# Kernel tuning notes

Hardware: AMD Instinct MI355X
Metric: run time of the kernel (lower is better)

The kernel has to match this reference:

```python
import jax, jax.numpy as jnp
import numpy as np

LAYERS = [1024, 2048, 1024]
OPTIONS = 4
BATCH = 2048


def setup_inputs() -> dict:
    key = jax.random.key(0)
    k_x, k_idx, k_w1, k_w2 = jax.random.split(key, 4)
    x = jax.random.normal(k_x, (BATCH, LAYERS[0]), dtype=jnp.float32)
    idx = jax.random.randint(k_idx, (BATCH,), 0, OPTIONS, dtype=jnp.int64)
    # xavier-normal-ish scaled weights per layer: shape [options, in, out]
    std1 = float(np.sqrt(2.0 / (LAYERS[0] * LAYERS[1] + OPTIONS * LAYERS[1])))
    std2 = float(np.sqrt(2.0 / (LAYERS[1] * LAYERS[2] + OPTIONS * LAYERS[2])))
    W1 = jax.random.normal(k_w1, (OPTIONS, LAYERS[0], LAYERS[1]), dtype=jnp.float32) * std1
    b1 = jnp.zeros((OPTIONS, LAYERS[1]), dtype=jnp.float32)
    W2 = jax.random.normal(k_w2, (OPTIONS, LAYERS[1], LAYERS[2]), dtype=jnp.float32) * std2
    b2 = jnp.zeros((OPTIONS, LAYERS[2]), dtype=jnp.float32)
    return {"x": x, "idx": idx, "W1": W1, "b1": b1, "W2": W2, "b2": b2}


def reference(x, idx, W1, b1, W2, b2):
    # Original: torch.bmm(x[:,None,:], W[idx]) + b[zeros_like(idx)]
    # Equivalent math without materializing the [B, in, out] gathered weights:
    # compute all options densely, then select per-sample option with idx.
    # NOTE: bias is ALWAYS option 0 (faithful to the original's zeros_like(idx)).
    def layer(h, W, b):
        h_all = jnp.einsum('bi,oij->boj', h, W)  # [B, O, out]
        h_sel = jnp.take_along_axis(h_all, idx[:, None, None], axis=1)[:, 0, :]  # [B, out]
        return h_sel + b[0][None, :]

    h = layer(x, W1, b1)
    out = layer(h, W2, b2)
    return out
```

## Files before the change

kernel.cpp:

```cpp
#include <hip/hip_runtime.h>
#include <stdint.h>

typedef __bf16 bf16x8 __attribute__((ext_vector_type(8)));
typedef float f32x4 __attribute__((ext_vector_type(4)));
typedef unsigned short u16;
typedef const __attribute__((address_space(1))) void* as1_cvp;
typedef __attribute__((address_space(3))) void* as3_vp;

__device__ __forceinline__ u16 f2bf(float f) {
  union { float f; unsigned u; } v; v.f = f;
  unsigned r = v.u + 0x7fffu + ((v.u >> 16) & 1u);
  return (u16)(r >> 16);
}

__global__ __launch_bounds__(256) void hist_perm_kernel(
    const int* __restrict__ idx, int n, int* __restrict__ starts,
    int* __restrict__ perm, int* __restrict__ tmap128,
    int* __restrict__ tmap64) {
  __shared__ int cnt[4][256];
  __shared__ int gtot[4], gstart[4];
  const int t = threadIdx.x;
  const int rpt = (n + 255) >> 8;
  const int base = t * rpt;
  int c[4] = {0, 0, 0, 0};
  for (int j = 0; j < rpt; ++j) {
    const int i = base + j;
    if (i < n) c[idx[i] & 3]++;
  }
  #pragma unroll
  for (int g = 0; g < 4; ++g) cnt[g][t] = c[g];
  __syncthreads();

  const int w = t >> 6, l = t & 63;
  {
    const int s0 = cnt[w][l * 4 + 0], s1 = cnt[w][l * 4 + 1];
    const int s2 = cnt[w][l * 4 + 2], s3 = cnt[w][l * 4 + 3];
    const int sum = s0 + s1 + s2 + s3;
    int sc = sum;
    #pragma unroll
    for (int d = 1; d < 64; d <<= 1) {
      const int o = __shfl_up(sc, d, 64);
      if (l >= d) sc += o;
    }
    const int ex = sc - sum;
    cnt[w][l * 4 + 0] = ex;
    cnt[w][l * 4 + 1] = ex + s0;
    cnt[w][l * 4 + 2] = ex + s0 + s1;
    cnt[w][l * 4 + 3] = ex + s0 + s1 + s2;
    if (l == 63) gtot[w] = sc;
  }
  __syncthreads();

  if (t == 0) {
    int s = 0, nt128 = 0, nt64 = 0;
    for (int g = 0; g < 4; ++g) {
      gstart[g] = s;
      starts[g] = s;
      const int cg = gtot[g];
      for (int j = 0; j < cg; j += 128) tmap128[nt128++] = (g << 28) | (s + j);
      for (int j = 0; j < cg; j += 64)  tmap64[nt64++]  = (g << 28) | (s + j);
      s += cg;
    }
    starts[4] = s;
    while (nt128 < 20) tmap128[nt128++] = -1;
    while (nt64 < 40)  tmap64[nt64++]  = -1;
  }
  __syncthreads();

  int run[4] = {0, 0, 0, 0};
  for (int j = 0; j < rpt; ++j) {
    const int i = base + j;
    if (i < n) {
      const int g = idx[i] & 3;
      perm[gstart[g] + cnt[g][t] + run[g]] = i;
      run[g]++;
    }
  }
}

__global__ __launch_bounds__(256) void prep_kernel(
    const float* __restrict__ W1, u16* __restrict__ W1T,
    const float* __restrict__ W2, u16* __restrict__ W2T,
    const float* __restrict__ x, const int* __restrict__ perm,
    u16* __restrict__ Xs) {
  __shared__ float tile[64][65];
  int bid = blockIdx.x;
  if (bid >= 4096) {
    const int p = bid - 4096;
    const int b = perm[p];
    const float4 v = ((const float4*)(x + (size_t)b * 1024))[threadIdx.x];
    ushort4 u;
    u.x = f2bf(v.x); u.y = f2bf(v.y); u.z = f2bf(v.z); u.w = f2bf(v.w);
    ((ushort4*)(Xs + (size_t)p * 1024))[threadIdx.x] = u;
    return;
  }
  const float* W; u16* WT; int K, N, tx, ty, o;
  if (bid < 2048) {
    W = W1; WT = W1T; K = 1024; N = 2048;
    o = bid >> 9; const int t = bid & 511; tx = t & 31; ty = t >> 5;
  } else {
    bid -= 2048;
    W = W2; WT = W2T; K = 2048; N = 1024;
    o = bid >> 9; const int t = bid & 511; tx = t & 15; ty = t >> 4;
  }
  const float* Wo = W + (size_t)o * K * N;
  u16* WTo = WT + (size_t)o * N * K;
  const int k0 = ty * 64, n0 = tx * 64;
  const int rr = threadIdx.x >> 4, cc = threadIdx.x & 15;
  #pragma unroll
  for (int j = 0; j < 4; ++j) {
    const int r = j * 16 + rr;
    const float4 v = *(const float4*)(Wo + (size_t)(k0 + r) * N + n0 + cc * 4);
    tile[r][cc * 4 + 0] = v.x; tile[r][cc * 4 + 1] = v.y;
    tile[r][cc * 4 + 2] = v.z; tile[r][cc * 4 + 3] = v.w;
  }
  __syncthreads();
  #pragma unroll
  for (int j = 0; j < 4; ++j) {
    const int nrow = j * 16 + rr;
    ushort4 u;
    u.x = f2bf(tile[cc * 4 + 0][nrow]);
    u.y = f2bf(tile[cc * 4 + 1][nrow]);
    u.z = f2bf(tile[cc * 4 + 2][nrow]);
    u.w = f2bf(tile[cc * 4 + 3][nrow]);
    *(ushort4*)(WTo + (size_t)(n0 + nrow) * K + k0 + cc * 4) = u;
  }
}

template <int EPI, int TM, int NT_PAD, int KT, int NN, int NTN>
__global__ __launch_bounds__(256, 2) void gemm_kernel(
    const u16* __restrict__ A, const u16* __restrict__ BT,
    const float* __restrict__ bias, const int* __restrict__ starts,
    const int* __restrict__ tmap, const int* __restrict__ perm,
    u16* __restrict__ outH, float* __restrict__ outF) {
  constexpr int MR = TM / 32;
  constexpr int ABUF = TM * 128;
  constexpr int BSTR = ABUF + 16384;
  __shared__ char smem[2 * BSTR];

  const int nwg = NT_PAD * NTN;
  const int q = nwg >> 3;
  const int bid = blockIdx.x;
  const int swz = (bid & 7) * q + (bid >> 3);
  const int tile = swz % NT_PAD;
  const int n_t = swz / NT_PAD;

  const int tm = tmap[tile];
  if (tm < 0) return;
  const int o = tm >> 28;
  const int m_start = tm & 0x0FFFFFFF;
  const int g1 = starts[o + 1];
  const int n_start = n_t * 128;
  const u16* Bo = BT + (size_t)o * NN * KT;

  const int tid = threadIdx.x;
  const int w = tid >> 6;
  const int l = tid & 63;
  const int wm = w >> 1, wn = w & 1;
  const int l8 = l & 7, ld8 = l >> 3;

  const int src_unit = l8 ^ (ld8 & 7);

  const u16* pA[MR];
  #pragma unroll
  for (int j = 0; j < MR; ++j) {
    int r = m_start + (j * 4 + w) * 8 + ld8;
    if (r >= g1) r = g1 - 1;
    pA[j] = A + (size_t)r * KT + src_unit * 8;
  }
  const u16* pB[4];
  #pragma unroll
  for (int j = 0; j < 4; ++j) {
    const int nr = n_start + (j * 4 + w) * 8 + ld8;
    pB[j] = Bo + (size_t)nr * KT + src_unit * 8;
  }

#define STAGE(dst_off)                                                         \
  {                                                                            \
    _Pragma("unroll")                                                          \
    for (int j = 0; j < MR; ++j)                                               \
      __builtin_amdgcn_global_load_lds((as1_cvp)pA[j],                         \
          (as3_vp)(smem + (dst_off) + (j * 4 + w) * 1024), 16, 0, 0);          \
    _Pragma("unroll")                                                          \
    for (int j = 0; j < 4; ++j)                                                \
      __builtin_amdgcn_global_load_lds((as1_cvp)pB[j],                         \
          (as3_vp)(smem + (dst_off) + ABUF + (j * 4 + w) * 1024), 16, 0, 0);   \
    _Pragma("unroll") for (int j = 0; j < MR; ++j) pA[j] += 64;                \
    _Pragma("unroll") for (int j = 0; j < 4; ++j) pB[j] += 64;                 \
  }

  const int lrow = l & 15;
  const int lx = l & 7;
  const int lu = l >> 4;
  int offA[MR][2], offB[4][2];
  #pragma unroll
  for (int a = 0; a < MR; ++a)
    #pragma unroll
    for (int kk = 0; kk < 2; ++kk)
      offA[a][kk] = (wm * (TM / 2) + a * 16 + lrow) * 128 + (((kk * 4 + lu) ^ lx) << 4);
  #pragma unroll
  for (int b = 0; b < 4; ++b)
    #pragma unroll
    for (int kk = 0; kk < 2; ++kk)
      offB[b][kk] = (wn * 64 + b * 16 + lrow) * 128 + (((kk * 4 + lu) ^ lx) << 4);

  f32x4 acc[MR][4] = {};

  const int nK = KT >> 6;
  STAGE(0);
  for (int kt = 0; kt < nK; ++kt) {
    const int cur = (kt & 1) * BSTR;
    if (kt + 1 < nK) {
      STAGE(BSTR - cur);
      if constexpr (TM == 128)
        asm volatile("s_waitcnt vmcnt(8)" ::: "memory");
      else
        asm volatile("s_waitcnt vmcnt(6)" ::: "memory");
    } else {
      asm volatile("s_waitcnt vmcnt(0)" ::: "memory");
    }
    __builtin_amdgcn_s_barrier();

    bf16x8 af[MR][2], bfr[4][2];
    #pragma unroll
    for (int a = 0; a < MR; ++a)
      #pragma unroll
      for (int kk = 0; kk < 2; ++kk)
        af[a][kk] = *(const bf16x8*)(smem + cur + offA[a][kk]);
    #pragma unroll
    for (int b = 0; b < 4; ++b)
      #pragma unroll
      for (int kk = 0; kk < 2; ++kk)
        bfr[b][kk] = *(const bf16x8*)(smem + cur + ABUF + offB[b][kk]);
    asm volatile("s_waitcnt lgkmcnt(0)" ::: "memory");
    __builtin_amdgcn_s_barrier();

    __builtin_amdgcn_s_setprio(1);
    #pragma unroll
    for (int kk = 0; kk < 2; ++kk)
      #pragma unroll
      for (int a = 0; a < MR; ++a)
        #pragma unroll
        for (int b = 0; b < 4; ++b)
          acc[a][b] = __builtin_amdgcn_mfma_f32_16x16x32_bf16(af[a][kk], bfr[b][kk], acc[a][b], 0, 0, 0);
    __builtin_amdgcn_s_setprio(0);
  }
#undef STAGE

  const int col_l = l & 15;
  const int row_l = (l >> 4) << 2;
  #pragma unroll
  for (int a = 0; a < MR; ++a) {
    #pragma unroll
    for (int b = 0; b < 4; ++b) {
      const int n = n_start + wn * 64 + b * 16 + col_l;
      const float bv = bias[n];
      #pragma unroll
      for (int r = 0; r < 4; ++r) {
        const int p = m_start + wm * (TM / 2) + a * 16 + row_l + r;
        if (p < g1) {
          if (EPI == 0) {
            outH[(size_t)p * NN + n] = f2bf(acc[a][b][r] + bv);
          } else {
            outF[(size_t)perm[p] * NN + n] = acc[a][b][r] + bv;
          }
        }
      }
    }
  }
}

extern "C" void kernel_launch(void* const* d_in, const int* in_sizes, int n_in,
                              void* d_out, int out_size, void* d_ws, size_t ws_size,
                              hipStream_t stream) {
  (void)n_in; (void)out_size; (void)ws_size;
  const float* x   = (const float*)d_in[0];
  const int*   idx = (const int*)d_in[1];
  const float* W1  = (const float*)d_in[2];
  const float* b1  = (const float*)d_in[3];
  const float* W2  = (const float*)d_in[4];
  const float* b2  = (const float*)d_in[5];
  float* out = (float*)d_out;

  const int B = in_sizes[1];

  char* ws = (char*)d_ws;
  u16* W1T     = (u16*)(ws);
  u16* W2T     = (u16*)(ws + 16777216);
  u16* Xs      = (u16*)(ws + 33554432);
  u16* Hs      = (u16*)(ws + 37748736);
  int* perm    = (int*)(ws + 46137344);
  int* starts  = (int*)(ws + 46137344 + 8192);
  int* tmap128 = starts + 64;
  int* tmap64  = starts + 128;

  hist_perm_kernel<<<1, 256, 0, stream>>>(idx, B, starts, perm, tmap128, tmap64);
  prep_kernel<<<4096 + B, 256, 0, stream>>>(W1, W1T, W2, W2T, x, perm, Xs);

  gemm_kernel<0, 128, 20, 1024, 2048, 16><<<320, 256, 0, stream>>>(
      Xs, W1T, b1, starts, tmap128, perm, Hs, nullptr);
  gemm_kernel<1, 64, 40, 2048, 1024, 8><<<320, 256, 0, stream>>>(
      Hs, W2T, b2, starts, tmap64, perm, nullptr, out);
}
```

Baseline: 78.90 us.

## Use 64x128 tiles with 2-wave blocks for both grouped GEMMs

Both grouped GEMMs now use one configuration: 128-thread blocks of two waves, 64-row M tiles and 128-column N tiles, with each wave owning a 64x64 sub-tile. The first GEMM moves from 128-row tiles to 64-row tiles, which doubles its grid to 640 blocks and reduces padding waste at the group boundaries. The 128-row tile map is removed. In exchange, fewer waves per block have to hide latency, and B-tile reuse across M drops in the first layer, so each weight tile is fetched more often.

```diff
diff --git a/kernel.cpp b/kernel.cpp
--- a/kernel.cpp
+++ b/kernel.cpp
@@ -15,8 +15,7 @@
 
 __global__ __launch_bounds__(256) void hist_perm_kernel(
     const int* __restrict__ idx, int n, int* __restrict__ starts,
-    int* __restrict__ perm, int* __restrict__ tmap128,
-    int* __restrict__ tmap64) {
+    int* __restrict__ perm, int* __restrict__ tmap64) {
   __shared__ int cnt[4][256];
   __shared__ int gtot[4], gstart[4];
   const int t = threadIdx.x;
@@ -52,18 +51,16 @@
   __syncthreads();
 
   if (t == 0) {
-    int s = 0, nt128 = 0, nt64 = 0;
+    int s = 0, nt64 = 0;
     for (int g = 0; g < 4; ++g) {
       gstart[g] = s;
       starts[g] = s;
       const int cg = gtot[g];
-      for (int j = 0; j < cg; j += 128) tmap128[nt128++] = (g << 28) | (s + j);
-      for (int j = 0; j < cg; j += 64)  tmap64[nt64++]  = (g << 28) | (s + j);
+      for (int j = 0; j < cg; j += 64) tmap64[nt64++] = (g << 28) | (s + j);
       s += cg;
     }
     starts[4] = s;
-    while (nt128 < 20) tmap128[nt128++] = -1;
-    while (nt64 < 40)  tmap64[nt64++]  = -1;
+    while (nt64 < 40) tmap64[nt64++] = -1;
   }
   __syncthreads();
 
@@ -127,14 +124,13 @@
   }
 }
 
-template <int EPI, int TM, int NT_PAD, int KT, int NN, int NTN>
-__global__ __launch_bounds__(256, 2) void gemm_kernel(
+template <int EPI, int NT_PAD, int KT, int NN, int NTN>
+__global__ __launch_bounds__(128, 2) void gemm_kernel(
     const u16* __restrict__ A, const u16* __restrict__ BT,
     const float* __restrict__ bias, const int* __restrict__ starts,
     const int* __restrict__ tmap, const int* __restrict__ perm,
     u16* __restrict__ outH, float* __restrict__ outF) {
-  constexpr int MR = TM / 32;
-  constexpr int ABUF = TM * 128;
+  constexpr int ABUF = 8192;
   constexpr int BSTR = ABUF + 16384;
   __shared__ char smem[2 * BSTR];
 
@@ -156,55 +152,54 @@
   const int tid = threadIdx.x;
   const int w = tid >> 6;
   const int l = tid & 63;
-  const int wm = w >> 1, wn = w & 1;
   const int l8 = l & 7, ld8 = l >> 3;
 
-  const int src_unit = l8 ^ (ld8 & 7);
-
-  const u16* pA[MR];
-  #pragma unroll
-  for (int j = 0; j < MR; ++j) {
-    int r = m_start + (j * 4 + w) * 8 + ld8;
+  const int src_unit = l8 ^ ld8;
+
+  const u16* pA[4];
+  #pragma unroll
+  for (int j = 0; j < 4; ++j) {
+    int r = m_start + (w * 4 + j) * 8 + ld8;
     if (r >= g1) r = g1 - 1;
     pA[j] = A + (size_t)r * KT + src_unit * 8;
   }
-  const u16* pB[4];
-  #pragma unroll
-  for (int j = 0; j < 4; ++j) {
-    const int nr = n_start + (j * 4 + w) * 8 + ld8;
+  const u16* pB[8];
+  #pragma unroll
+  for (int j = 0; j < 8; ++j) {
+    const int nr = n_start + (w * 8 + j) * 8 + ld8;
     pB[j] = Bo + (size_t)nr * KT + src_unit * 8;
   }
 
 #define STAGE(dst_off)                                                         \
   {                                                                            \
     _Pragma("unroll")                                                          \
-    for (int j = 0; j < MR; ++j)                                               \
+    for (int j = 0; j < 4; ++j)                                                \
       __builtin_amdgcn_global_load_lds((as1_cvp)pA[j],                         \
-          (as3_vp)(smem + (dst_off) + (j * 4 + w) * 1024), 16, 0, 0);          \
+          (as3_vp)(smem + (dst_off) + (w * 4 + j) * 1024), 16, 0, 0);          \
     _Pragma("unroll")                                                          \
-    for (int j = 0; j < 4; ++j)                                                \
+    for (int j = 0; j < 8; ++j)                                                \
       __builtin_amdgcn_global_load_lds((as1_cvp)pB[j],                         \
-          (as3_vp)(smem + (dst_off) + ABUF + (j * 4 + w) * 1024), 16, 0, 0);   \
-    _Pragma("unroll") for (int j = 0; j < MR; ++j) pA[j] += 64;                \
-    _Pragma("unroll") for (int j = 0; j < 4; ++j) pB[j] += 64;                 \
+          (as3_vp)(smem + (dst_off) + ABUF + (w * 8 + j) * 1024), 16, 0, 0);   \
+    _Pragma("unroll") for (int j = 0; j < 4; ++j) pA[j] += 64;                 \
+    _Pragma("unroll") for (int j = 0; j < 8; ++j) pB[j] += 64;                 \
   }
 
   const int lrow = l & 15;
   const int lx = l & 7;
   const int lu = l >> 4;
-  int offA[MR][2], offB[4][2];
-  #pragma unroll
-  for (int a = 0; a < MR; ++a)
+  int offA[4][2], offB[4][2];
+  #pragma unroll
+  for (int a = 0; a < 4; ++a)
     #pragma unroll
     for (int kk = 0; kk < 2; ++kk)
-      offA[a][kk] = (wm * (TM / 2) + a * 16 + lrow) * 128 + (((kk * 4 + lu) ^ lx) << 4);
+      offA[a][kk] = (a * 16 + lrow) * 128 + (((kk * 4 + lu) ^ lx) << 4);
   #pragma unroll
   for (int b = 0; b < 4; ++b)
     #pragma unroll
     for (int kk = 0; kk < 2; ++kk)
-      offB[b][kk] = (wn * 64 + b * 16 + lrow) * 128 + (((kk * 4 + lu) ^ lx) << 4);
-
-  f32x4 acc[MR][4] = {};
+      offB[b][kk] = (w * 64 + b * 16 + lrow) * 128 + (((kk * 4 + lu) ^ lx) << 4);
+
+  f32x4 acc[4][4] = {};
 
   const int nK = KT >> 6;
   STAGE(0);
@@ -212,18 +207,15 @@
     const int cur = (kt & 1) * BSTR;
     if (kt + 1 < nK) {
       STAGE(BSTR - cur);
-      if constexpr (TM == 128)
-        asm volatile("s_waitcnt vmcnt(8)" ::: "memory");
-      else
-        asm volatile("s_waitcnt vmcnt(6)" ::: "memory");
+      asm volatile("s_waitcnt vmcnt(12)" ::: "memory");
     } else {
       asm volatile("s_waitcnt vmcnt(0)" ::: "memory");
     }
     __builtin_amdgcn_s_barrier();
 
-    bf16x8 af[MR][2], bfr[4][2];
-    #pragma unroll
-    for (int a = 0; a < MR; ++a)
+    bf16x8 af[4][2], bfr[4][2];
+    #pragma unroll
+    for (int a = 0; a < 4; ++a)
       #pragma unroll
       for (int kk = 0; kk < 2; ++kk)
         af[a][kk] = *(const bf16x8*)(smem + cur + offA[a][kk]);
@@ -239,7 +231,7 @@
     #pragma unroll
     for (int kk = 0; kk < 2; ++kk)
       #pragma unroll
-      for (int a = 0; a < MR; ++a)
+      for (int a = 0; a < 4; ++a)
         #pragma unroll
         for (int b = 0; b < 4; ++b)
           acc[a][b] = __builtin_amdgcn_mfma_f32_16x16x32_bf16(af[a][kk], bfr[b][kk], acc[a][b], 0, 0, 0);
@@ -250,14 +242,14 @@
   const int col_l = l & 15;
   const int row_l = (l >> 4) << 2;
   #pragma unroll
-  for (int a = 0; a < MR; ++a) {
+  for (int a = 0; a < 4; ++a) {
     #pragma unroll
     for (int b = 0; b < 4; ++b) {
-      const int n = n_start + wn * 64 + b * 16 + col_l;
+      const int n = n_start + w * 64 + b * 16 + col_l;
       const float bv = bias[n];
       #pragma unroll
       for (int r = 0; r < 4; ++r) {
-        const int p = m_start + wm * (TM / 2) + a * 16 + row_l + r;
+        const int p = m_start + a * 16 + row_l + r;
         if (p < g1) {
           if (EPI == 0) {
             outH[(size_t)p * NN + n] = f2bf(acc[a][b][r] + bv);
@@ -291,14 +283,13 @@
   u16* Hs      = (u16*)(ws + 37748736);
   int* perm    = (int*)(ws + 46137344);
   int* starts  = (int*)(ws + 46137344 + 8192);
-  int* tmap128 = starts + 64;
-  int* tmap64  = starts + 128;
-
-  hist_perm_kernel<<<1, 256, 0, stream>>>(idx, B, starts, perm, tmap128, tmap64);
+  int* tmap64  = starts + 64;
+
+  hist_perm_kernel<<<1, 256, 0, stream>>>(idx, B, starts, perm, tmap64);
   prep_kernel<<<4096 + B, 256, 0, stream>>>(W1, W1T, W2, W2T, x, perm, Xs);
 
-  gemm_kernel<0, 128, 20, 1024, 2048, 16><<<320, 256, 0, stream>>>(
-      Xs, W1T, b1, starts, tmap128, perm, Hs, nullptr);
-  gemm_kernel<1, 64, 40, 2048, 1024, 8><<<320, 256, 0, stream>>>(
+  gemm_kernel<0, 40, 1024, 2048, 16><<<640, 128, 0, stream>>>(
+      Xs, W1T, b1, starts, tmap64, perm, Hs, nullptr);
+  gemm_kernel<1, 40, 2048, 1024, 8><<<320, 128, 0, stream>>>(
       Hs, W2T, b2, starts, tmap64, perm, nullptr, out);
 }
```

Result: slower. 86.50 us (+9.6%).

## Overlap W2 transpose-convert with first GEMM in a combined launch

Applied to the files above, without the earlier changes.

Splits the prep kernel so only the W1 transpose and the x gather run before GEMM1. The W2 fp32-to-bf16 transpose now runs as extra workgroups inside the GEMM1 launch, so it can fill the CUs left idle by GEMM1's 320 workgroups. Transpose tiles are also remapped so that consecutive tiles land on the same XCD, aiming at better L2 locality. The cost is that the GEMM1 kernel now reserves a fixed 64KB of shared memory, which could lower occupancy, and its workgroups compete with the transpose blocks for bandwidth.

```diff
diff --git a/kernel.cpp b/kernel.cpp
--- a/kernel.cpp
+++ b/kernel.cpp
@@ -30,7 +30,6 @@
   #pragma unroll
   for (int g = 0; g < 4; ++g) cnt[g][t] = c[g];
   __syncthreads();
-
   const int w = t >> 6, l = t & 63;
   {
     const int s0 = cnt[w][l * 4 + 0], s1 = cnt[w][l * 4 + 1];
@@ -50,7 +49,6 @@
     if (l == 63) gtot[w] = sc;
   }
   __syncthreads();
-
   if (t == 0) {
     int s = 0, nt128 = 0, nt64 = 0;
     for (int g = 0; g < 4; ++g) {
@@ -66,7 +64,6 @@
     while (nt64 < 40)  tmap64[nt64++]  = -1;
   }
   __syncthreads();
-
   int run[4] = {0, 0, 0, 0};
   for (int j = 0; j < rpt; ++j) {
     const int i = base + j;
@@ -78,31 +75,9 @@
   }
 }
 
-__global__ __launch_bounds__(256) void prep_kernel(
-    const float* __restrict__ W1, u16* __restrict__ W1T,
-    const float* __restrict__ W2, u16* __restrict__ W2T,
-    const float* __restrict__ x, const int* __restrict__ perm,
-    u16* __restrict__ Xs) {
-  __shared__ float tile[64][65];
-  int bid = blockIdx.x;
-  if (bid >= 4096) {
-    const int p = bid - 4096;
-    const int b = perm[p];
-    const float4 v = ((const float4*)(x + (size_t)b * 1024))[threadIdx.x];
-    ushort4 u;
-    u.x = f2bf(v.x); u.y = f2bf(v.y); u.z = f2bf(v.z); u.w = f2bf(v.w);
-    ((ushort4*)(Xs + (size_t)p * 1024))[threadIdx.x] = u;
-    return;
-  }
-  const float* W; u16* WT; int K, N, tx, ty, o;
-  if (bid < 2048) {
-    W = W1; WT = W1T; K = 1024; N = 2048;
-    o = bid >> 9; const int t = bid & 511; tx = t & 31; ty = t >> 5;
-  } else {
-    bid -= 2048;
-    W = W2; WT = W2T; K = 2048; N = 1024;
-    o = bid >> 9; const int t = bid & 511; tx = t & 15; ty = t >> 4;
-  }
+__device__ __forceinline__ void wtrans_body(
+    float (*tile)[65], const float* __restrict__ W, u16* __restrict__ WT,
+    int K, int N, int tx, int ty, int o) {
   const float* Wo = W + (size_t)o * K * N;
   u16* WTo = WT + (size_t)o * N * K;
   const int k0 = ty * 64, n0 = tx * 64;
@@ -127,8 +102,31 @@
   }
 }
 
+__global__ __launch_bounds__(256) void w1t_gather_kernel(
+    const float* __restrict__ W1, u16* __restrict__ W1T,
+    const float* __restrict__ x, const int* __restrict__ perm,
+    u16* __restrict__ Xs) {
+  __shared__ float tile[64][65];
+  const int bid = blockIdx.x;
+  if (bid >= 2048) {
+    const int p = bid - 2048;
+    const int b = perm[p];
+    const float4 v = ((const float4*)(x + (size_t)b * 1024))[threadIdx.x];
+    ushort4 u;
+    u.x = f2bf(v.x); u.y = f2bf(v.y); u.z = f2bf(v.z); u.w = f2bf(v.w);
+    ((ushort4*)(Xs + (size_t)p * 1024))[threadIdx.x] = u;
+    return;
+  }
+  const int xcd = bid & 7, i = bid >> 3;
+  const int tx = (xcd << 2) | (i & 3);
+  const int ty = (i >> 2) & 15;
+  const int o = i >> 6;
+  wtrans_body(tile, W1, W1T, 1024, 2048, tx, ty, o);
+}
+
 template <int EPI, int TM, int NT_PAD, int KT, int NN, int NTN>
-__global__ __launch_bounds__(256, 2) void gemm_kernel(
+__device__ __forceinline__ void gemm_body(
+    char* smem, int bid,
     const u16* __restrict__ A, const u16* __restrict__ BT,
     const float* __restrict__ bias, const int* __restrict__ starts,
     const int* __restrict__ tmap, const int* __restrict__ perm,
@@ -136,11 +134,9 @@
   constexpr int MR = TM / 32;
   constexpr int ABUF = TM * 128;
   constexpr int BSTR = ABUF + 16384;
-  __shared__ char smem[2 * BSTR];
 
   const int nwg = NT_PAD * NTN;
   const int q = nwg >> 3;
-  const int bid = blockIdx.x;
   const int swz = (bid & 7) * q + (bid >> 3);
   const int tile = swz % NT_PAD;
   const int n_t = swz / NT_PAD;
@@ -270,6 +266,36 @@
   }
 }
 
+__global__ __launch_bounds__(256, 2) void gemm1_w2t_kernel(
+    const u16* __restrict__ Xs, const u16* __restrict__ W1T,
+    const float* __restrict__ b1, const int* __restrict__ starts,
+    const int* __restrict__ tmap128, u16* __restrict__ Hs,
+    const float* __restrict__ W2, u16* __restrict__ W2T) {
+  __shared__ char smem[65536];
+  const int bid = blockIdx.x;
+  if (bid < 320) {
+    gemm_body<0, 128, 20, 1024, 2048, 16>(
+        smem, bid, Xs, W1T, b1, starts, tmap128, nullptr, Hs, nullptr);
+  } else {
+    const int b = bid - 320;
+    const int xcd = b & 7, i = b >> 3;
+    const int tx = (xcd << 1) | (i & 1);
+    const int ty = (i >> 1) & 31;
+    const int o = i >> 6;
+    wtrans_body((float(*)[65])smem, W2, W2T, 2048, 1024, tx, ty, o);
+  }
+}
+
+__global__ __launch_bounds__(256, 2) void gemm2_kernel(
+    const u16* __restrict__ Hs, const u16* __restrict__ W2T,
+    const float* __restrict__ b2, const int* __restrict__ starts,
+    const int* __restrict__ tmap64, const int* __restrict__ perm,
+    float* __restrict__ out) {
+  __shared__ char smem[49152];
+  gemm_body<1, 64, 40, 2048, 1024, 8>(
+      smem, blockIdx.x, Hs, W2T, b2, starts, tmap64, perm, nullptr, out);
+}
+
 extern "C" void kernel_launch(void* const* d_in, const int* in_sizes, int n_in,
                               void* d_out, int out_size, void* d_ws, size_t ws_size,
                               hipStream_t stream) {
@@ -295,10 +321,8 @@
   int* tmap64  = starts + 128;
 
   hist_perm_kernel<<<1, 256, 0, stream>>>(idx, B, starts, perm, tmap128, tmap64);
-  prep_kernel<<<4096 + B, 256, 0, stream>>>(W1, W1T, W2, W2T, x, perm, Xs);
-
-  gemm_kernel<0, 128, 20, 1024, 2048, 16><<<320, 256, 0, stream>>>(
-      Xs, W1T, b1, starts, tmap128, perm, Hs, nullptr);
-  gemm_kernel<1, 64, 40, 2048, 1024, 8><<<320, 256, 0, stream>>>(
-      Hs, W2T, b2, starts, tmap64, perm, nullptr, out);
-}
+  w1t_gather_kernel<<<2048 + B, 256, 0, stream>>>(W1, W1T, x, perm, Xs);
+  gemm1_w2t_kernel<<<320 + 2048, 256, 0, stream>>>(
+      Xs, W1T, b1, starts, tmap128, Hs, W2, W2T);
+  gemm2_kernel<<<320, 256, 0, stream>>>(Hs, W2T, b2, starts, tmap64, perm, out);
+}
```

Result: faster. 72.73 us (-7.8%).

## Fuse weight transpose and bf16 conversion into GEMM B-tile loading

Applied to the files above, without the earlier changes.

Drops the separate prep pass that transposed and converted both fp32 weight tensors to bf16 in workspace. Each GEMM now loads fp32 weight tiles into registers, packs them to bf16 with v_cvt_pk_bf16_f32, and writes them transposed into a re-swizzled LDS layout. This removes a full read/write round trip of the weights, but each GEMM tile re-reads fp32 weights (twice the bytes), and the main loop now waits vmcnt(0) each iteration, which weakens the overlap between loads and MFMA.

```diff
diff --git a/kernel.cpp b/kernel.cpp
--- a/kernel.cpp
+++ b/kernel.cpp
@@ -4,6 +4,7 @@
 typedef __bf16 bf16x8 __attribute__((ext_vector_type(8)));
 typedef float f32x4 __attribute__((ext_vector_type(4)));
 typedef unsigned short u16;
+typedef unsigned int u32;
 typedef const __attribute__((address_space(1))) void* as1_cvp;
 typedef __attribute__((address_space(3))) void* as3_vp;
 
@@ -12,6 +13,13 @@
   unsigned r = v.u + 0x7fffu + ((v.u >> 16) & 1u);
   return (u16)(r >> 16);
 }
+
+__device__ __forceinline__ float f4g(const float4& v, int j) {
+  return j == 0 ? v.x : j == 1 ? v.y : j == 2 ? v.z : v.w;
+}
+
+#define CVTPK(dst, a, b) \
+  asm("v_cvt_pk_bf16_f32 %0, %1, %2" : "=v"(dst) : "v"(a), "v"(b))
 
 __global__ __launch_bounds__(256) void hist_perm_kernel(
     const int* __restrict__ idx, int n, int* __restrict__ starts,
@@ -30,7 +38,6 @@
   #pragma unroll
   for (int g = 0; g < 4; ++g) cnt[g][t] = c[g];
   __syncthreads();
-
   const int w = t >> 6, l = t & 63;
   {
     const int s0 = cnt[w][l * 4 + 0], s1 = cnt[w][l * 4 + 1];
@@ -50,7 +57,6 @@
     if (l == 63) gtot[w] = sc;
   }
   __syncthreads();
-
   if (t == 0) {
     int s = 0, nt128 = 0, nt64 = 0;
     for (int g = 0; g < 4; ++g) {
@@ -66,7 +72,6 @@
     while (nt64 < 40)  tmap64[nt64++]  = -1;
   }
   __syncthreads();
-
   int run[4] = {0, 0, 0, 0};
   for (int j = 0; j < rpt; ++j) {
     const int i = base + j;
@@ -78,58 +83,20 @@
   }
 }
 
-__global__ __launch_bounds__(256) void prep_kernel(
-    const float* __restrict__ W1, u16* __restrict__ W1T,
-    const float* __restrict__ W2, u16* __restrict__ W2T,
+__global__ __launch_bounds__(256) void gather_kernel(
     const float* __restrict__ x, const int* __restrict__ perm,
     u16* __restrict__ Xs) {
-  __shared__ float tile[64][65];
-  int bid = blockIdx.x;
-  if (bid >= 4096) {
-    const int p = bid - 4096;
-    const int b = perm[p];
-    const float4 v = ((const float4*)(x + (size_t)b * 1024))[threadIdx.x];
-    ushort4 u;
-    u.x = f2bf(v.x); u.y = f2bf(v.y); u.z = f2bf(v.z); u.w = f2bf(v.w);
-    ((ushort4*)(Xs + (size_t)p * 1024))[threadIdx.x] = u;
-    return;
-  }
-  const float* W; u16* WT; int K, N, tx, ty, o;
-  if (bid < 2048) {
-    W = W1; WT = W1T; K = 1024; N = 2048;
-    o = bid >> 9; const int t = bid & 511; tx = t & 31; ty = t >> 5;
-  } else {
-    bid -= 2048;
-    W = W2; WT = W2T; K = 2048; N = 1024;
-    o = bid >> 9; const int t = bid & 511; tx = t & 15; ty = t >> 4;
-  }
-  const float* Wo = W + (size_t)o * K * N;
-  u16* WTo = WT + (size_t)o * N * K;
-  const int k0 = ty * 64, n0 = tx * 64;
-  const int rr = threadIdx.x >> 4, cc = threadIdx.x & 15;
-  #pragma unroll
-  for (int j = 0; j < 4; ++j) {
-    const int r = j * 16 + rr;
-    const float4 v = *(const float4*)(Wo + (size_t)(k0 + r) * N + n0 + cc * 4);
-    tile[r][cc * 4 + 0] = v.x; tile[r][cc * 4 + 1] = v.y;
-    tile[r][cc * 4 + 2] = v.z; tile[r][cc * 4 + 3] = v.w;
-  }
-  __syncthreads();
-  #pragma unroll
-  for (int j = 0; j < 4; ++j) {
-    const int nrow = j * 16 + rr;
-    ushort4 u;
-    u.x = f2bf(tile[cc * 4 + 0][nrow]);
-    u.y = f2bf(tile[cc * 4 + 1][nrow]);
-    u.z = f2bf(tile[cc * 4 + 2][nrow]);
-    u.w = f2bf(tile[cc * 4 + 3][nrow]);
-    *(ushort4*)(WTo + (size_t)(n0 + nrow) * K + k0 + cc * 4) = u;
-  }
+  const int p = blockIdx.x;
+  const int b = perm[p];
+  const float4 v = ((const float4*)(x + (size_t)b * 1024))[threadIdx.x];
+  ushort4 u;
+  u.x = f2bf(v.x); u.y = f2bf(v.y); u.z = f2bf(v.z); u.w = f2bf(v.w);
+  ((ushort4*)(Xs + (size_t)p * 1024))[threadIdx.x] = u;
 }
 
 template <int EPI, int TM, int NT_PAD, int KT, int NN, int NTN>
-__global__ __launch_bounds__(256, 2) void gemm_kernel(
-    const u16* __restrict__ A, const u16* __restrict__ BT,
+__global__ __launch_bounds__(256, 2) void gemm_direct(
+    const u16* __restrict__ A, const float* __restrict__ W,
     const float* __restrict__ bias, const int* __restrict__ starts,
     const int* __restrict__ tmap, const int* __restrict__ perm,
     u16* __restrict__ outH, float* __restrict__ outF) {
@@ -151,7 +118,7 @@
   const int m_start = tm & 0x0FFFFFFF;
   const int g1 = starts[o + 1];
   const int n_start = n_t * 128;
-  const u16* Bo = BT + (size_t)o * NN * KT;
+  const float* Wo = W + (size_t)o * KT * NN;
 
   const int tid = threadIdx.x;
   const int w = tid >> 6;
@@ -160,7 +127,6 @@
   const int l8 = l & 7, ld8 = l >> 3;
 
   const int src_unit = l8 ^ (ld8 & 7);
-
   const u16* pA[MR];
   #pragma unroll
   for (int j = 0; j < MR; ++j) {
@@ -168,25 +134,34 @@
     if (r >= g1) r = g1 - 1;
     pA[j] = A + (size_t)r * KT + src_unit * 8;
   }
-  const u16* pB[4];
-  #pragma unroll
-  for (int j = 0; j < 4; ++j) {
-    const int nr = n_start + (j * 4 + w) * 8 + ld8;
-    pB[j] = Bo + (size_t)nr * KT + src_unit * 8;
-  }
-
-#define STAGE(dst_off)                                                         \
+
+#define STAGE_A(dst_off)                                                       \
   {                                                                            \
     _Pragma("unroll")                                                          \
     for (int j = 0; j < MR; ++j)                                               \
       __builtin_amdgcn_global_load_lds((as1_cvp)pA[j],                         \
           (as3_vp)(smem + (dst_off) + (j * 4 + w) * 1024), 16, 0, 0);          \
+    _Pragma("unroll") for (int j = 0; j < MR; ++j) pA[j] += 64;                \
+  }
+
+  const int nloc = (l & 31) * 4;
+  const int kloc = w * 16 + (l >> 5) * 8;
+  const float* pBf = Wo + (size_t)kloc * NN + n_start + nloc;
+  const int u_ = (kloc >> 3);
+  int wrB[4];
+  #pragma unroll
+  for (int j = 0; j < 4; ++j) {
+    const int n = nloc + j;
+    wrB[j] = n * 128 + ((u_ ^ (n & 7) ^ ((n >> 2) & 7)) << 4);
+  }
+
+  float4 ld[8];
+#define LOADB()                                                                \
+  {                                                                            \
     _Pragma("unroll")                                                          \
-    for (int j = 0; j < 4; ++j)                                                \
-      __builtin_amdgcn_global_load_lds((as1_cvp)pB[j],                         \
-          (as3_vp)(smem + (dst_off) + ABUF + (j * 4 + w) * 1024), 16, 0, 0);   \
-    _Pragma("unroll") for (int j = 0; j < MR; ++j) pA[j] += 64;                \
-    _Pragma("unroll") for (int j = 0; j < 4; ++j) pB[j] += 64;                 \
+    for (int i = 0; i < 8; ++i)                                                \
+      ld[i] = *(const float4*)(pBf + (size_t)i * NN);                          \
+    pBf += (size_t)64 * NN;                                                    \
   }
 
   const int lrow = l & 15;
@@ -199,26 +174,38 @@
     for (int kk = 0; kk < 2; ++kk)
       offA[a][kk] = (wm * (TM / 2) + a * 16 + lrow) * 128 + (((kk * 4 + lu) ^ lx) << 4);
   #pragma unroll
-  for (int b = 0; b < 4; ++b)
+  for (int b = 0; b < 4; ++b) {
+    const int row = wn * 64 + b * 16 + lrow;
     #pragma unroll
     for (int kk = 0; kk < 2; ++kk)
-      offB[b][kk] = (wn * 64 + b * 16 + lrow) * 128 + (((kk * 4 + lu) ^ lx) << 4);
+      offB[b][kk] = row * 128 +
+          (((kk * 4 + lu) ^ (row & 7) ^ ((row >> 2) & 7)) << 4);
+  }
 
   f32x4 acc[MR][4] = {};
 
-  const int nK = KT >> 6;
-  STAGE(0);
-  for (int kt = 0; kt < nK; ++kt) {
-    const int cur = (kt & 1) * BSTR;
-    if (kt + 1 < nK) {
-      STAGE(BSTR - cur);
-      if constexpr (TM == 128)
-        asm volatile("s_waitcnt vmcnt(8)" ::: "memory");
-      else
-        asm volatile("s_waitcnt vmcnt(6)" ::: "memory");
-    } else {
-      asm volatile("s_waitcnt vmcnt(0)" ::: "memory");
-    }
+  constexpr int nK = KT >> 6;
+  LOADB();
+  STAGE_A(0);
+  for (int t = 0; t < nK; ++t) {
+    const int cur = (t & 1) * BSTR;
+    asm volatile("s_waitcnt vmcnt(0)" ::: "memory");
+
+    #pragma unroll
+    for (int j = 0; j < 4; ++j) {
+      u32 w0, w1, w2, w3;
+      CVTPK(w0, f4g(ld[0], j), f4g(ld[1], j));
+      CVTPK(w1, f4g(ld[2], j), f4g(ld[3], j));
+      CVTPK(w2, f4g(ld[4], j), f4g(ld[5], j));
+      CVTPK(w3, f4g(ld[6], j), f4g(ld[7], j));
+      uint4 pk; pk.x = w0; pk.y = w1; pk.z = w2; pk.w = w3;
+      *(uint4*)(smem + cur + ABUF + wrB[j]) = pk;
+    }
+    if (t + 1 < nK) {
+      LOADB();
+      STAGE_A(BSTR - cur);
+    }
+    asm volatile("s_waitcnt lgkmcnt(0)" ::: "memory");
     __builtin_amdgcn_s_barrier();
 
     bf16x8 af[MR][2], bfr[4][2];
@@ -245,7 +232,8 @@
           acc[a][b] = __builtin_amdgcn_mfma_f32_16x16x32_bf16(af[a][kk], bfr[b][kk], acc[a][b], 0, 0, 0);
     __builtin_amdgcn_s_setprio(0);
   }
-#undef STAGE
+#undef LOADB
+#undef STAGE_A
 
   const int col_l = l & 15;
   const int row_l = (l >> 4) << 2;
@@ -285,20 +273,18 @@
   const int B = in_sizes[1];
 
   char* ws = (char*)d_ws;
-  u16* W1T     = (u16*)(ws);
-  u16* W2T     = (u16*)(ws + 16777216);
-  u16* Xs      = (u16*)(ws + 33554432);
-  u16* Hs      = (u16*)(ws + 37748736);
-  int* perm    = (int*)(ws + 46137344);
-  int* starts  = (int*)(ws + 46137344 + 8192);
+  u16* Xs      = (u16*)(ws);
+  u16* Hs      = (u16*)(ws + 4194304);
+  int* perm    = (int*)(ws + 12582912);
+  int* starts  = (int*)(ws + 12582912 + 8192);
   int* tmap128 = starts + 64;
   int* tmap64  = starts + 128;
 
   hist_perm_kernel<<<1, 256, 0, stream>>>(idx, B, starts, perm, tmap128, tmap64);
-  prep_kernel<<<4096 + B, 256, 0, stream>>>(W1, W1T, W2, W2T, x, perm, Xs);
-
-  gemm_kernel<0, 128, 20, 1024, 2048, 16><<<320, 256, 0, stream>>>(
-      Xs, W1T, b1, starts, tmap128, perm, Hs, nullptr);
-  gemm_kernel<1, 64, 40, 2048, 1024, 8><<<320, 256, 0, stream>>>(
-      Hs, W2T, b2, starts, tmap64, perm, nullptr, out);
-}
+  gather_kernel<<<B, 256, 0, stream>>>(x, perm, Xs);
+
+  gemm_direct<0, 128, 20, 1024, 2048, 16><<<320, 256, 0, stream>>>(
+      Xs, W1, b1, starts, tmap128, perm, Hs, nullptr);
+  gemm_direct<1, 64, 40, 2048, 1024, 8><<<320, 256, 0, stream>>>(
+      Hs, W2, b2, starts, tmap64, perm, nullptr, out);
+}
```

After: 77.29 us. 1.02x faster.
